# Performance work log

Measured on AMD Instinct MI355X. Metric: run time of the kernel, lower is better.

## Reference

```python
import jax, jax.numpy as jnp
import numpy as np

N, E, R = 50000, 640000, 3
EMB, HID, NCLS, G = 64, 128, 4, 512
NSHAPE, NCOLOR = 16, 16
IN_DIM = 2 * EMB + 1


def setup_inputs() -> dict:
    key = jax.random.key(0)
    ks = jax.random.split(key, 16)
    gl = lambda k, shp, fan: (jax.random.normal(k, shp, jnp.float32) / np.sqrt(fan)).astype(jnp.float32)
    return {
        "pos": jax.random.normal(ks[0], (N, 1), jnp.float32),
        "shape_id": jax.random.randint(ks[1], (N,), 0, NSHAPE),
        "color_id": jax.random.randint(ks[2], (N,), 0, NCOLOR),
        "edge_index": jax.random.randint(ks[3], (2, E), 0, N),
        "edge_type": jax.random.randint(ks[4], (E,), 0, R),
        "batch": jnp.sort(jax.random.randint(ks[5], (N,), 0, G)),
        "shape_emb_w": jax.random.normal(ks[6], (NSHAPE, EMB), jnp.float32),
        "color_emb_w": jax.random.normal(ks[7], (NCOLOR, EMB), jnp.float32),
        "W1": gl(ks[8], (R, IN_DIM, HID), IN_DIM),
        "root1": gl(ks[9], (IN_DIM, HID), IN_DIM),
        "b1": jnp.zeros((HID,), jnp.float32),
        "W2": gl(ks[10], (R, HID, HID), HID),
        "root2": gl(ks[11], (HID, HID), HID),
        "b2": jnp.zeros((HID,), jnp.float32),
        "lin_w": gl(ks[12], (HID, NCLS), HID),
        "lin_b": jnp.zeros((NCLS,), jnp.float32),
    }


def rgcn_conv(x, edge_index, edge_type, W, root, b):
    """PyG RGCNConv: per-relation mean aggregation of source features,
    then per-relation linear, summed; plus root transform and bias."""
    n = x.shape[0]
    src, dst = edge_index[0], edge_index[1]
    seg = edge_type * n + dst                          # [E] relation-major segment id
    msg = x[src]                                       # [E, d] gather
    sums = jax.ops.segment_sum(msg, seg, num_segments=R * n).reshape(R, n, -1)
    cnt = jax.ops.segment_sum(jnp.ones((E,), x.dtype), seg, num_segments=R * n).reshape(R, n, 1)
    mean = sums / jnp.maximum(cnt, 1.0)                # [R, n, d]
    return jnp.einsum('rnd,rdh->nh', mean, W) + x @ root + b


def reference(pos, shape_id, color_id, edge_index, edge_type, batch,
              shape_emb_w, color_emb_w, W1, root1, b1, W2, root2, b2, lin_w, lin_b):
    x = jnp.concatenate([shape_emb_w[shape_id], color_emb_w[color_id], pos], axis=1)  # [N, IN_DIM]
    x = jax.nn.relu(rgcn_conv(x, edge_index, edge_type, W1, root1, b1))
    # dropout is identity at inference
    x = jax.nn.relu(rgcn_conv(x, edge_index, edge_type, W2, root2, b2))
    # global mean pool per graph
    s = jax.ops.segment_sum(x, batch, num_segments=G)
    c = jax.ops.segment_sum(jnp.ones((x.shape[0],), x.dtype), batch, num_segments=G)[:, None]
    pooled = s / jnp.maximum(c, 1.0)                   # [G, HID]
    return pooled @ lin_w + lin_b                      # [G, NCLS]
```

## Files before the change

### kernel.cpp

```cpp
#include <hip/hip_runtime.h>
#include <hip/hip_bf16.h>

#define NNODE 50000
#define NEDGE 640000
#define NREL  3
#define HIDD  128
#define GNUM  512
#define K1M   128
#define K2    512
#define NB    196

typedef float  f32x4   __attribute__((ext_vector_type(4)));
typedef short  vshort8 __attribute__((ext_vector_type(8)));

#define SWZ(row, kb) ((((kb) ^ (((row) >> 1) & 3)) << 3))

__device__ __forceinline__ short bf16_rne(float f) {
    unsigned u = __float_as_uint(f);
    return (short)((u + 0x7FFFu + ((u >> 16) & 1u)) >> 16);
}

__global__ void build_tabs_kernel(const float* __restrict__ shape_w,
                                  const float* __restrict__ color_w,
                                  const float* __restrict__ W1,
                                  const float* __restrict__ root1,
                                  const float* __restrict__ W2,
                                  const float* __restrict__ root2,
                                  short* __restrict__ B1th,
                                  float* __restrict__ rootTab,
                                  short* __restrict__ Bt_hi) {
    int idx = blockIdx.x * blockDim.x + threadIdx.x;
    if (idx < K1M * 128) {
        int k = idx >> 7, n = idx & 127;
        float v = 0.f;
        if (k < 99) {
            int r = k / 33, j = k - r * 33;
            const float* Wsrc = W1 + (size_t)r * 129 * 128;
            if (j < 16) {
                for (int e = 0; e < 64; ++e) v += shape_w[j * 64 + e] * Wsrc[e * 128 + n];
            } else if (j < 32) {
                int c = j - 16;
                for (int e = 0; e < 64; ++e) v += color_w[c * 64 + e] * Wsrc[(64 + e) * 128 + n];
            } else {
                v = Wsrc[128 * 128 + n];
            }
        }
        B1th[(size_t)n * K1M + k] = bf16_rne(v);
        return;
    }
    int idx2 = idx - K1M * 128;
    if (idx2 < 33 * 128) {
        int h = idx2 & 127, j = idx2 >> 7;
        float v;
        if (j < 16) {
            v = 0.f;
            for (int e = 0; e < 64; ++e) v += shape_w[j * 64 + e] * root1[e * 128 + h];
        } else if (j < 32) {
            int c = j - 16;
            v = 0.f;
            for (int e = 0; e < 64; ++e) v += color_w[c * 64 + e] * root1[(64 + e) * 128 + h];
        } else {
            v = root1[128 * 128 + h];
        }
        rootTab[j * 128 + h] = v;
        return;
    }
    int idx3 = idx2 - 33 * 128;
    if (idx3 >= K2 * 128) return;
    int k = idx3 >> 7, n = idx3 & 127;
    float v = (k < 384) ? W2[idx3] : root2[idx3 - 384 * 128];
    Bt_hi[(size_t)n * K2 + k] = bf16_rne(v);
}

__global__ void count_nf_kernel(const int* __restrict__ ei, const int* __restrict__ et,
                                const int* __restrict__ shape_id, const int* __restrict__ color_id,
                                const float* __restrict__ pos,
                                int* __restrict__ cnt, int* __restrict__ rank,
                                int2* __restrict__ nf) {
    int e = blockIdx.x * blockDim.x + threadIdx.x;
    if (e < NNODE) nf[e] = make_int2(shape_id[e] | (color_id[e] << 8), __float_as_int(pos[e]));
    if (e >= NEDGE) return;
    int d = ei[NEDGE + e], r = et[e];
    rank[e] = atomicAdd(&cnt[d * 3 + r], 1);
}

__global__ void scan_partial_kernel(const int* __restrict__ cnt, int* __restrict__ partial) {
    __shared__ int sh[256];
    int t = threadIdx.x, i = blockIdx.x * 256 + t;
    int v = (i < NNODE) ? cnt[3 * i] + cnt[3 * i + 1] + cnt[3 * i + 2] : 0;
    sh[t] = v; __syncthreads();
    for (int o = 128; o > 0; o >>= 1) { if (t < o) sh[t] += sh[t + o]; __syncthreads(); }
    if (t == 0) partial[blockIdx.x] = sh[0];
}

__global__ void scan_final_kernel(const int* __restrict__ cnt, const int* __restrict__ partial,
                                  int* __restrict__ offs3, float* __restrict__ rcnt) {
    __shared__ int shp[256];
    __shared__ int sh[256];
    int t = threadIdx.x, i = blockIdx.x * 256 + t;
    int pv = (t < NB) ? partial[t] : 0;
    shp[t] = pv; __syncthreads();
    for (int o = 1; o < 256; o <<= 1) {
        int x = (t >= o) ? shp[t - o] : 0; __syncthreads();
        shp[t] += x; __syncthreads();
    }
    int blockOff = (blockIdx.x > 0) ? shp[blockIdx.x - 1] : 0;
    int c0 = 0, c1 = 0, c2 = 0;
    if (i < NNODE) { c0 = cnt[3 * i]; c1 = cnt[3 * i + 1]; c2 = cnt[3 * i + 2]; }
    int v = c0 + c1 + c2;
    sh[t] = v; __syncthreads();
    for (int o = 1; o < 256; o <<= 1) {
        int x = (t >= o) ? sh[t - o] : 0; __syncthreads();
        sh[t] += x; __syncthreads();
    }
    int exc = sh[t] - v + blockOff;
    if (i < NNODE) {
        offs3[3 * i]     = exc;
        offs3[3 * i + 1] = exc + c0;
        offs3[3 * i + 2] = exc + c0 + c1;
        float4 rc = make_float4(1.f / fmaxf((float)c0, 1.f), 1.f / fmaxf((float)c1, 1.f),
                                1.f / fmaxf((float)c2, 1.f), 1.f);
        *(float4*)&rcnt[i * 4] = rc;
    }
    if (blockIdx.x == 0 && t == 0) offs3[3 * NNODE] = NEDGE;
}

__global__ void fill_kernel(const int* __restrict__ ei, const int* __restrict__ et,
                            const int* __restrict__ rank, const int* __restrict__ offs3,
                            int* __restrict__ sorted) {
    int e = blockIdx.x * blockDim.x + threadIdx.x;
    if (e >= NEDGE) return;
    int s = ei[e], d = ei[NEDGE + e], r = et[e];
    int p = offs3[d * 3 + r] + rank[e];
    sorted[p] = s | (r << 16);
}

__global__ __launch_bounds__(256) void hist1_kernel(const int* __restrict__ offs3,
                                                    const int* __restrict__ sorted,
                                                    const int2* __restrict__ nf,
                                                    const float* __restrict__ rcnt,
                                                    unsigned short* __restrict__ A1h) {
    __shared__ float hist[4][3 * 34];
    int lane = threadIdx.x & 63;
    int wv   = threadIdx.x >> 6;
    int d    = (blockIdx.x << 2) + wv;
    float* hf = hist[wv];
    if (lane < 51) { hf[lane] = 0.f; hf[lane + 51] = 0.f; }
    if (d < NNODE) {
        int beg = offs3[3 * d], end = offs3[3 * d + 3];
        for (int i = beg + lane; i < end; i += 64) {
            int w = sorted[i];
            int s = w & 0xFFFF, r = (w >> 16) & 3;
            int2 f = nf[s];
            atomicAdd(&hf[r * 34 + (f.x & 0xFF)], 1.f);
            atomicAdd(&hf[r * 34 + 16 + (f.x >> 8)], 1.f);
            atomicAdd(&hf[r * 34 + 32], __int_as_float(f.y));
        }
#pragma unroll
        for (int half = 0; half < 2; ++half) {
            int slot = lane + half * 64;
            float v = 0.f;
            if (slot < 99) {
                int r = slot / 33;
                v = hf[r * 34 + (slot - r * 33)] * rcnt[d * 4 + r];
            }
            A1h[(size_t)d * K1M + slot] = (unsigned short)bf16_rne(v);
        }
    }
}

__global__ __launch_bounds__(256) void aggregate_kernel(const int* __restrict__ offs3,
                                                        const int* __restrict__ sorted,
                                                        const float* __restrict__ rcnt,
                                                        unsigned short* __restrict__ A2h) {
    int lane = threadIdx.x & 63;
    int d = (blockIdx.x << 2) + (threadIdx.x >> 6);
    if (d >= NNODE) return;
    int b0  = __builtin_amdgcn_readfirstlane(offs3[3 * d]);
    int b1  = __builtin_amdgcn_readfirstlane(offs3[3 * d + 1]);
    int b2  = __builtin_amdgcn_readfirstlane(offs3[3 * d + 2]);
    int end = __builtin_amdgcn_readfirstlane(offs3[3 * d + 3]);
    const unsigned* xp = (const unsigned*)A2h;
    float a00 = 0.f, a01 = 0.f, a10 = 0.f, a11 = 0.f, a20 = 0.f, a21 = 0.f;
#define AGG_ACC(ii, x) {                                            \
        float lo_ = __uint_as_float((x) << 16);                     \
        float hi_ = __uint_as_float((x) & 0xFFFF0000u);             \
        if ((ii) >= b2)      { a20 += lo_; a21 += hi_; }            \
        else if ((ii) >= b1) { a10 += lo_; a11 += hi_; }            \
        else                 { a00 += lo_; a01 += hi_; } }
#define AGG_LD(j)  unsigned x##j = xp[((size_t)(unsigned)(sorted[i + j] & 0xFFFF) << 8) + 192 + lane]
    int i = b0;
    for (; i + 8 <= end; i += 8) {
        AGG_LD(0); AGG_LD(1); AGG_LD(2); AGG_LD(3);
        AGG_LD(4); AGG_LD(5); AGG_LD(6); AGG_LD(7);
        AGG_ACC(i, x0); AGG_ACC(i + 1, x1); AGG_ACC(i + 2, x2); AGG_ACC(i + 3, x3);
        AGG_ACC(i + 4, x4); AGG_ACC(i + 5, x5); AGG_ACC(i + 6, x6); AGG_ACC(i + 7, x7);
    }
    for (; i + 4 <= end; i += 4) {
        AGG_LD(0); AGG_LD(1); AGG_LD(2); AGG_LD(3);
        AGG_ACC(i, x0); AGG_ACC(i + 1, x1); AGG_ACC(i + 2, x2); AGG_ACC(i + 3, x3);
    }
    for (; i < end; ++i) {
        AGG_LD(0);
        AGG_ACC(i, x0);
    }
#undef AGG_LD
#undef AGG_ACC
    float rc0 = rcnt[d * 4 + 0], rc1 = rcnt[d * 4 + 1], rc2 = rcnt[d * 4 + 2];
    size_t base = (size_t)d * 512 + (lane << 1);
#define AGG_OUT(vA, vB, rel) {                                        \
        unsigned short h0_ = (unsigned short)bf16_rne(vA);            \
        unsigned short h1_ = (unsigned short)bf16_rne(vB);            \
        *(unsigned*)&A2h[base + (rel) * 128] = (unsigned)h0_ | ((unsigned)h1_ << 16); }
    AGG_OUT(a00 * rc0, a01 * rc0, 0);
    AGG_OUT(a10 * rc1, a11 * rc1, 1);
    AGG_OUT(a20 * rc2, a21 * rc2, 2);
#undef AGG_OUT
}

__global__ __launch_bounds__(256) void gemm1_mfma_kernel(
    const unsigned short* __restrict__ A1h,
    const short* __restrict__ B1th,
    const int* __restrict__ shape_id, const int* __restrict__ color_id,
    const float* __restrict__ pos, const float* __restrict__ rootTab,
    const float* __restrict__ bias,
    unsigned short* __restrict__ A2h) {
    __shared__ short Ah[64][32];
    __shared__ short Bh[128][32];
    const int t    = threadIdx.x;
    const int lane = t & 63;
    const int w    = t >> 6;
    const int wm   = w >> 1, wn = w & 1;
    const int bm0  = blockIdx.x * 64;
    const int lr   = lane & 15, lk = lane >> 4;
    const int sr = t >> 2, skb = t & 3;
    int gra = bm0 + sr; if (gra >= NNODE) gra = NNODE - 1;
    f32x4 acc[2][4] = {};
    for (int kt = 0; kt < K1M; kt += 32) {
        vshort8 avh = *(const vshort8*)&A1h[(size_t)gra * K1M + kt + skb * 8];
        vshort8 bvh0 = *(const vshort8*)&B1th[(size_t)sr * K1M + kt + skb * 8];
        vshort8 bvh1 = *(const vshort8*)&B1th[(size_t)(sr + 64) * K1M + kt + skb * 8];
        __syncthreads();
        *(vshort8*)&Ah[sr][SWZ(sr, skb)]           = avh;
        *(vshort8*)&Bh[sr][SWZ(sr, skb)]           = bvh0;
        *(vshort8*)&Bh[sr + 64][SWZ(sr + 64, skb)] = bvh1;
        __syncthreads();
        vshort8 afh[2], bfh[4];
#pragma unroll
        for (int mf = 0; mf < 2; ++mf) {
            int row = wm * 32 + mf * 16 + lr;
            afh[mf] = *(const vshort8*)&Ah[row][SWZ(row, lk)];
        }
#pragma unroll
        for (int nf = 0; nf < 4; ++nf) {
            int row = wn * 64 + nf * 16 + lr;
            bfh[nf] = *(const vshort8*)&Bh[row][SWZ(row, lk)];
        }
#pragma unroll
        for (int mf = 0; mf < 2; ++mf)
#pragma unroll
            for (int nf = 0; nf < 4; ++nf)
                acc[mf][nf] = __builtin_amdgcn_mfma_f32_16x16x32_bf16(afh[mf], bfh[nf], acc[mf][nf], 0, 0, 0);
    }
#pragma unroll
    for (int mf = 0; mf < 2; ++mf) {
        int mb = bm0 + wm * 32 + mf * 16 + (lane >> 4) * 4;
#pragma unroll
        for (int r = 0; r < 4; ++r) {
            int gm = mb + r;
            if (gm >= NNODE) continue;
            int sid = shape_id[gm], cid = color_id[gm];
            float pv = pos[gm];
#pragma unroll
            for (int nf = 0; nf < 4; ++nf) {
                int n = wn * 64 + nf * 16 + lr;
                float v = acc[mf][nf][r] + rootTab[sid * 128 + n] + rootTab[(16 + cid) * 128 + n]
                        + pv * rootTab[32 * 128 + n] + bias[n];
                A2h[(size_t)gm * 512 + 384 + n] = (unsigned short)bf16_rne(fmaxf(v, 0.f));
            }
        }
    }
}

__global__ __launch_bounds__(256) void gemm2_mfma_kernel(
    const unsigned short* __restrict__ A2h,
    const short* __restrict__ Bt_hi,
    const float* __restrict__ bias,
    unsigned short* __restrict__ x2b) {
    __shared__ short Ah[64][32];
    __shared__ short Bh[128][32];
    const int t    = threadIdx.x;
    const int lane = t & 63;
    const int w    = t >> 6;
    const int wm   = w >> 1, wn = w & 1;
    const int bm0  = blockIdx.x * 64;
    const int lr   = lane & 15, lk = lane >> 4;
    const int sr = t >> 2, skb = t & 3;
    int gra = bm0 + sr; if (gra >= NNODE) gra = NNODE - 1;
    f32x4 acc[2][4] = {};
    for (int kt = 0; kt < K2; kt += 32) {
        vshort8 avh = *(const vshort8*)&A2h[(size_t)gra * K2 + kt + skb * 8];
        vshort8 bvh0 = *(const vshort8*)&Bt_hi[(size_t)sr * K2 + kt + skb * 8];
        vshort8 bvh1 = *(const vshort8*)&Bt_hi[(size_t)(sr + 64) * K2 + kt + skb * 8];
        __syncthreads();
        *(vshort8*)&Ah[sr][SWZ(sr, skb)]           = avh;
        *(vshort8*)&Bh[sr][SWZ(sr, skb)]           = bvh0;
        *(vshort8*)&Bh[sr + 64][SWZ(sr + 64, skb)] = bvh1;
        __syncthreads();
        vshort8 afh[2], bfh[4];
#pragma unroll
        for (int mf = 0; mf < 2; ++mf) {
            int row = wm * 32 + mf * 16 + lr;
            afh[mf] = *(const vshort8*)&Ah[row][SWZ(row, lk)];
        }
#pragma unroll
        for (int nf = 0; nf < 4; ++nf) {
            int row = wn * 64 + nf * 16 + lr;
            bfh[nf] = *(const vshort8*)&Bh[row][SWZ(row, lk)];
        }
#pragma unroll
        for (int mf = 0; mf < 2; ++mf)
#pragma unroll
            for (int nf = 0; nf < 4; ++nf)
                acc[mf][nf] = __builtin_amdgcn_mfma_f32_16x16x32_bf16(afh[mf], bfh[nf], acc[mf][nf], 0, 0, 0);
    }
#pragma unroll
    for (int mf = 0; mf < 2; ++mf) {
        int mb = bm0 + wm * 32 + mf * 16 + (lane >> 4) * 4;
#pragma unroll
        for (int nf = 0; nf < 4; ++nf) {
            int n = wn * 64 + nf * 16 + lr;
            float bn = bias[n];
#pragma unroll
            for (int r = 0; r < 4; ++r) {
                int gm = mb + r;
                if (gm < NNODE)
                    x2b[(size_t)gm * HIDD + n] =
                        (unsigned short)bf16_rne(fmaxf(acc[mf][nf][r] + bn, 0.f));
            }
        }
    }
}

__global__ void pool_kernel(const unsigned short* __restrict__ x2b, const int* __restrict__ batch,
                            float* __restrict__ pooled, float* __restrict__ cntg) {
    const int CH = 64;
    int h  = threadIdx.x;
    int n0 = blockIdx.x * CH;
    if (n0 >= NNODE) return;
    int n1 = min(n0 + CH, NNODE);
    int cur = batch[n0];
    float acc = 0.f;
    int run = 0;
    for (int n = n0; n < n1; ++n) {
        int g = batch[n];
        if (g != cur) {
            atomicAdd(&pooled[cur * 128 + h], acc);
            if (h == 0) atomicAdd(&cntg[cur], (float)run);
            acc = 0.f; run = 0; cur = g;
        }
        acc += __uint_as_float((unsigned)x2b[(size_t)n * 128 + h] << 16);
        ++run;
    }
    atomicAdd(&pooled[cur * 128 + h], acc);
    if (h == 0) atomicAdd(&cntg[cur], (float)run);
}

__global__ void final_kernel(const float* __restrict__ pooled, const float* __restrict__ cntg,
                             const float* __restrict__ lin_w, const float* __restrict__ lin_b,
                             float* __restrict__ out) {
    int idx = blockIdx.x * blockDim.x + threadIdx.x;
    if (idx >= GNUM * 4) return;
    int g = idx >> 2, c = idx & 3;
    float dot = 0.f;
    for (int k = 0; k < 128; ++k) dot += pooled[g * 128 + k] * lin_w[k * 4 + c];
    out[idx] = dot / fmaxf(cntg[g], 1.f) + lin_b[c];
}

extern "C" void kernel_launch(void* const* d_in, const int* in_sizes, int n_in,
                              void* d_out, int out_size, void* d_ws, size_t ws_size,
                              hipStream_t stream) {
    const float* pos      = (const float*)d_in[0];
    const int*   shape_id = (const int*)d_in[1];
    const int*   color_id = (const int*)d_in[2];
    const int*   ei       = (const int*)d_in[3];
    const int*   et       = (const int*)d_in[4];
    const int*   batch    = (const int*)d_in[5];
    const float* shape_w  = (const float*)d_in[6];
    const float* color_w  = (const float*)d_in[7];
    const float* W1       = (const float*)d_in[8];
    const float* root1    = (const float*)d_in[9];
    const float* b1       = (const float*)d_in[10];
    const float* W2       = (const float*)d_in[11];
    const float* root2    = (const float*)d_in[12];
    const float* b2       = (const float*)d_in[13];
    const float* lin_w    = (const float*)d_in[14];
    const float* lin_b    = (const float*)d_in[15];
    float* out = (float*)d_out;

    char* p = (char*)d_ws;
    auto alloc = [&](size_t bytes) { char* r = p; p += (bytes + 255) & ~(size_t)255; return r; };
    int*   cnt     = (int*)alloc((size_t)NNODE * 3 * 4);
    unsigned short* A1h = (unsigned short*)alloc((size_t)NNODE * K1M * 2);
    float* rcntBuf = (float*)alloc((size_t)NNODE * 4 * 4);
    unsigned short* A2h = (unsigned short*)alloc((size_t)NNODE * K2 * 2);
    unsigned short* x2b = (unsigned short*)alloc((size_t)NNODE * 128 * 2);
    float* rootTab = (float*)alloc((size_t)33 * 128 * 4);
    short* B1th    = (short*)alloc((size_t)128 * K1M * 2);
    short* Bt_hi   = (short*)alloc((size_t)128 * K2 * 2);
    float* pooled  = (float*)alloc((size_t)GNUM * 128 * 4);
    float* cntg    = (float*)alloc((size_t)GNUM * 4);
    int2*  nfTab   = (int2*)alloc((size_t)NNODE * 8);
    char* xb = (char*)x2b;
    int* sorted  = (int*)(xb);
    int* offs3   = (int*)(xb + 2600960);
    int* rank    = (int*)(xb + 3201280);
    int* partial = (int*)(xb + 5761536);

    hipMemsetAsync(cnt,    0, (size_t)NNODE * 3 * 4, stream);
    hipMemsetAsync(pooled, 0, (size_t)GNUM * 128 * 4, stream);
    hipMemsetAsync(cntg,   0, (size_t)GNUM * 4, stream);

    build_tabs_kernel<<<(K1M * 128 + 33 * 128 + K2 * 128 + 255) / 256, 256, 0, stream>>>(
        shape_w, color_w, W1, root1, W2, root2, B1th, rootTab, Bt_hi);

    count_nf_kernel<<<(NEDGE + 255) / 256, 256, 0, stream>>>(
        ei, et, shape_id, color_id, pos, cnt, rank, nfTab);
    scan_partial_kernel<<<NB, 256, 0, stream>>>(cnt, partial);
    scan_final_kernel<<<NB, 256, 0, stream>>>(cnt, partial, offs3, rcntBuf);
    fill_kernel<<<(NEDGE + 255) / 256, 256, 0, stream>>>(ei, et, rank, offs3, sorted);

    hist1_kernel<<<(NNODE + 3) / 4, 256, 0, stream>>>(offs3, sorted, nfTab, rcntBuf, A1h);

    gemm1_mfma_kernel<<<(NNODE + 63) / 64, 256, 0, stream>>>(
        A1h, B1th, shape_id, color_id, pos, rootTab, b1, A2h);

    aggregate_kernel<<<(NNODE + 3) / 4, 256, 0, stream>>>(offs3, sorted, rcntBuf, A2h);

    gemm2_mfma_kernel<<<(NNODE + 63) / 64, 256, 0, stream>>>(
        A2h, Bt_hi, b2, x2b);

    pool_kernel<<<(NNODE + 63) / 64, 128, 0, stream>>>(x2b, batch, pooled, cntg);

    final_kernel<<<(GNUM * 4 + 255) / 256, 256, 0, stream>>>(
        pooled, cntg, lin_w, lin_b, out);
}
```

Baseline: 172.4 us.

## Fuse mean-pool into GEMM2 epilogue and fold memsets into existing kernels

GEMM2 now stages its ReLU output tile in LDS and reduces rows per graph directly into the pooled buffer with atomics. This removes the bf16 x2b write/read and the separate pool kernel. The per-graph node counts move into count_nf as integer atomics, and the three hipMemsetAsync calls become zeroing loops inside build_tabs and scan_partial. Pooling now sums fp32 values instead of bf16-rounded ones, and the LDS buffer grows to hold a 64x132 float tile, which may lower occupancy. The scratch buffers that used to alias x2b now get their own allocations.

```diff
diff --git a/kernel.cpp b/kernel.cpp
--- a/kernel.cpp
+++ b/kernel.cpp
@@ -28,8 +28,13 @@
                                   const float* __restrict__ root2,
                                   short* __restrict__ B1th,
                                   float* __restrict__ rootTab,
-                                  short* __restrict__ Bt_hi) {
+                                  short* __restrict__ Bt_hi,
+                                  int* __restrict__ cnt, int* __restrict__ cntgi) {
     int idx = blockIdx.x * blockDim.x + threadIdx.x;
+    const int NTH = ((K1M * 128 + 33 * 128 + K2 * 128 + 255) / 256) * 256;
+    for (int z = idx; z < NNODE * 3 + GNUM; z += NTH) {
+        if (z < NNODE * 3) cnt[z] = 0; else cntgi[z - NNODE * 3] = 0;
+    }
     if (idx < K1M * 128) {
         int k = idx >> 7, n = idx & 127;
         float v = 0.f;
@@ -74,19 +79,24 @@
 
 __global__ void count_nf_kernel(const int* __restrict__ ei, const int* __restrict__ et,
                                 const int* __restrict__ shape_id, const int* __restrict__ color_id,
-                                const float* __restrict__ pos,
+                                const float* __restrict__ pos, const int* __restrict__ batch,
                                 int* __restrict__ cnt, int* __restrict__ rank,
-                                int2* __restrict__ nf) {
+                                int2* __restrict__ nf, int* __restrict__ cntgi) {
     int e = blockIdx.x * blockDim.x + threadIdx.x;
-    if (e < NNODE) nf[e] = make_int2(shape_id[e] | (color_id[e] << 8), __float_as_int(pos[e]));
+    if (e < NNODE) {
+        nf[e] = make_int2(shape_id[e] | (color_id[e] << 8), __float_as_int(pos[e]));
+        atomicAdd(&cntgi[batch[e]], 1);
+    }
     if (e >= NEDGE) return;
     int d = ei[NEDGE + e], r = et[e];
     rank[e] = atomicAdd(&cnt[d * 3 + r], 1);
 }
 
-__global__ void scan_partial_kernel(const int* __restrict__ cnt, int* __restrict__ partial) {
+__global__ void scan_partial_kernel(const int* __restrict__ cnt, int* __restrict__ partial,
+                                    float* __restrict__ pooled) {
     __shared__ int sh[256];
     int t = threadIdx.x, i = blockIdx.x * 256 + t;
+    for (int z = i; z < GNUM * 128; z += NB * 256) pooled[z] = 0.f;
     int v = (i < NNODE) ? cnt[3 * i] + cnt[3 * i + 1] + cnt[3 * i + 2] : 0;
     sh[t] = v; __syncthreads();
     for (int o = 128; o > 0; o >>= 1) { if (t < o) sh[t] += sh[t + o]; __syncthreads(); }
@@ -286,9 +296,13 @@
     const unsigned short* __restrict__ A2h,
     const short* __restrict__ Bt_hi,
     const float* __restrict__ bias,
-    unsigned short* __restrict__ x2b) {
-    __shared__ short Ah[64][32];
-    __shared__ short Bh[128][32];
+    const int* __restrict__ batch,
+    float* __restrict__ pooled) {
+    __shared__ char smem[64 * 132 * 4 + 256];
+    short (*Ah)[32]   = (short(*)[32])smem;
+    short (*Bh)[32]   = (short(*)[32])(smem + 4096);
+    float (*Cst)[132] = (float(*)[132])smem;
+    int*  batchLDS    = (int*)(smem + 64 * 132 * 4);
     const int t    = threadIdx.x;
     const int lane = t & 63;
     const int w    = t >> 6;
@@ -324,49 +338,40 @@
             for (int nf = 0; nf < 4; ++nf)
                 acc[mf][nf] = __builtin_amdgcn_mfma_f32_16x16x32_bf16(afh[mf], bfh[nf], acc[mf][nf], 0, 0, 0);
     }
+    __syncthreads();
 #pragma unroll
     for (int mf = 0; mf < 2; ++mf) {
-        int mb = bm0 + wm * 32 + mf * 16 + (lane >> 4) * 4;
+        int rb = wm * 32 + mf * 16 + (lane >> 4) * 4;
 #pragma unroll
         for (int nf = 0; nf < 4; ++nf) {
             int n = wn * 64 + nf * 16 + lr;
             float bn = bias[n];
 #pragma unroll
-            for (int r = 0; r < 4; ++r) {
-                int gm = mb + r;
-                if (gm < NNODE)
-                    x2b[(size_t)gm * HIDD + n] =
-                        (unsigned short)bf16_rne(fmaxf(acc[mf][nf][r] + bn, 0.f));
+            for (int r = 0; r < 4; ++r)
+                Cst[rb + r][n] = fmaxf(acc[mf][nf][r] + bn, 0.f);
+        }
+    }
+    if (t < 64) batchLDS[t] = (bm0 + t < NNODE) ? batch[bm0 + t] : -1;
+    __syncthreads();
+    {
+        int col  = t & 127;
+        int rbeg = (t >> 7) * 32;
+        float accp = 0.f;
+        int cur = batchLDS[rbeg];
+        for (int rr = 0; rr < 32; ++rr) {
+            int row = rbeg + rr;
+            int g = batchLDS[row];
+            if (g != cur) {
+                if (cur >= 0) atomicAdd(&pooled[cur * 128 + col], accp);
+                accp = 0.f; cur = g;
             }
-        }
-    }
-}
-
-__global__ void pool_kernel(const unsigned short* __restrict__ x2b, const int* __restrict__ batch,
-                            float* __restrict__ pooled, float* __restrict__ cntg) {
-    const int CH = 64;
-    int h  = threadIdx.x;
-    int n0 = blockIdx.x * CH;
-    if (n0 >= NNODE) return;
-    int n1 = min(n0 + CH, NNODE);
-    int cur = batch[n0];
-    float acc = 0.f;
-    int run = 0;
-    for (int n = n0; n < n1; ++n) {
-        int g = batch[n];
-        if (g != cur) {
-            atomicAdd(&pooled[cur * 128 + h], acc);
-            if (h == 0) atomicAdd(&cntg[cur], (float)run);
-            acc = 0.f; run = 0; cur = g;
-        }
-        acc += __uint_as_float((unsigned)x2b[(size_t)n * 128 + h] << 16);
-        ++run;
-    }
-    atomicAdd(&pooled[cur * 128 + h], acc);
-    if (h == 0) atomicAdd(&cntg[cur], (float)run);
-}
-
-__global__ void final_kernel(const float* __restrict__ pooled, const float* __restrict__ cntg,
+            if (g >= 0) accp += Cst[row][col];
+        }
+        if (cur >= 0) atomicAdd(&pooled[cur * 128 + col], accp);
+    }
+}
+
+__global__ void final_kernel(const float* __restrict__ pooled, const int* __restrict__ cntgi,
                              const float* __restrict__ lin_w, const float* __restrict__ lin_b,
                              float* __restrict__ out) {
     int idx = blockIdx.x * blockDim.x + threadIdx.x;
@@ -374,7 +379,7 @@
     int g = idx >> 2, c = idx & 3;
     float dot = 0.f;
     for (int k = 0; k < 128; ++k) dot += pooled[g * 128 + k] * lin_w[k * 4 + c];
-    out[idx] = dot / fmaxf(cntg[g], 1.f) + lin_b[c];
+    out[idx] = dot / (float)max(cntgi[g], 1) + lin_b[c];
 }
 
 extern "C" void kernel_launch(void* const* d_in, const int* in_sizes, int n_in,
@@ -404,29 +409,23 @@
     unsigned short* A1h = (unsigned short*)alloc((size_t)NNODE * K1M * 2);
     float* rcntBuf = (float*)alloc((size_t)NNODE * 4 * 4);
     unsigned short* A2h = (unsigned short*)alloc((size_t)NNODE * K2 * 2);
-    unsigned short* x2b = (unsigned short*)alloc((size_t)NNODE * 128 * 2);
     float* rootTab = (float*)alloc((size_t)33 * 128 * 4);
     short* B1th    = (short*)alloc((size_t)128 * K1M * 2);
     short* Bt_hi   = (short*)alloc((size_t)128 * K2 * 2);
     float* pooled  = (float*)alloc((size_t)GNUM * 128 * 4);
-    float* cntg    = (float*)alloc((size_t)GNUM * 4);
+    int*   cntgi   = (int*)alloc((size_t)GNUM * 4);
     int2*  nfTab   = (int2*)alloc((size_t)NNODE * 8);
-    char* xb = (char*)x2b;
-    int* sorted  = (int*)(xb);
-    int* offs3   = (int*)(xb + 2600960);
-    int* rank    = (int*)(xb + 3201280);
-    int* partial = (int*)(xb + 5761536);
-
-    hipMemsetAsync(cnt,    0, (size_t)NNODE * 3 * 4, stream);
-    hipMemsetAsync(pooled, 0, (size_t)GNUM * 128 * 4, stream);
-    hipMemsetAsync(cntg,   0, (size_t)GNUM * 4, stream);
+    int*   sorted  = (int*)alloc((size_t)NEDGE * 4);
+    int*   offs3   = (int*)alloc((size_t)(3 * NNODE + 1) * 4);
+    int*   rank    = (int*)alloc((size_t)NEDGE * 4);
+    int*   partial = (int*)alloc((size_t)NB * 4);
 
     build_tabs_kernel<<<(K1M * 128 + 33 * 128 + K2 * 128 + 255) / 256, 256, 0, stream>>>(
-        shape_w, color_w, W1, root1, W2, root2, B1th, rootTab, Bt_hi);
+        shape_w, color_w, W1, root1, W2, root2, B1th, rootTab, Bt_hi, cnt, cntgi);
 
     count_nf_kernel<<<(NEDGE + 255) / 256, 256, 0, stream>>>(
-        ei, et, shape_id, color_id, pos, cnt, rank, nfTab);
-    scan_partial_kernel<<<NB, 256, 0, stream>>>(cnt, partial);
+        ei, et, shape_id, color_id, pos, batch, cnt, rank, nfTab, cntgi);
+    scan_partial_kernel<<<NB, 256, 0, stream>>>(cnt, partial, pooled);
     scan_final_kernel<<<NB, 256, 0, stream>>>(cnt, partial, offs3, rcntBuf);
     fill_kernel<<<(NEDGE + 255) / 256, 256, 0, stream>>>(ei, et, rank, offs3, sorted);
 
@@ -438,10 +437,8 @@
     aggregate_kernel<<<(NNODE + 3) / 4, 256, 0, stream>>>(offs3, sorted, rcntBuf, A2h);
 
     gemm2_mfma_kernel<<<(NNODE + 63) / 64, 256, 0, stream>>>(
-        A2h, Bt_hi, b2, x2b);
-
-    pool_kernel<<<(NNODE + 63) / 64, 128, 0, stream>>>(x2b, batch, pooled, cntg);
+        A2h, Bt_hi, b2, batch, pooled);
 
     final_kernel<<<(GNUM * 4 + 255) / 256, 256, 0, stream>>>(
-        pooled, cntg, lin_w, lin_b, out);
-}
+        pooled, cntgi, lin_w, lin_b, out);
+}
```

Result: no change. 170.3 us (-1.2%).
